# Optimization experiments

Measured on AMD Instinct MI355X. Metric: run time of the kernel, lower is better.

The kernel has to match this reference:

```python
import jax, jax.numpy as jnp
import numpy as np

N = 4096      # (num_domains+1) * batch_size
F_IN = 512    # nfeat
HID = 64      # nhid per head
H = 8         # nheads
ALPHA = 0.2   # leaky-relu negative slope
EDGE_P = 0.01 # adjacency density


def setup_inputs() -> dict:
    key = jax.random.key(0)
    k1, k2, k3, k4 = jax.random.split(key, 4)
    x = jax.random.normal(k1, (N, F_IN), dtype=jnp.float32)
    adj = (jax.random.uniform(k2, (N, N)) < EDGE_P).astype(jnp.float32)
    # ensure self-loops so every row has at least one valid edge for softmax
    adj = jnp.maximum(adj, jnp.eye(N, dtype=jnp.float32))
    W = jax.random.normal(k3, (H, F_IN, HID), dtype=jnp.float32) * 0.1
    a = jax.random.normal(k4, (H, 2 * HID), dtype=jnp.float32) * 0.1
    return {"x": x, "adj": adj, "W": W, "a": a}


def reference(x, adj, W, a):
    # Wh: [H, N, HID] -- per-head linear projection
    Wh = jnp.einsum('nf,hfd->hnd', x, W)
    # additive attention logits: e_ij = leakyrelu(a1.Wh_i + a2.Wh_j)
    e_src = jnp.einsum('hnd,hd->hn', Wh, a[:, :HID])   # [H, N]
    e_dst = jnp.einsum('hnd,hd->hn', Wh, a[:, HID:])   # [H, N]
    e = jax.nn.leaky_relu(e_src[:, :, None] + e_dst[:, None, :], ALPHA)  # [H, N, N]
    e = jnp.where(adj[None] > 0, e, jnp.float32(-9e15))
    att = jax.nn.softmax(e, axis=-1)                    # masked softmax over neighbors
    h = jnp.einsum('hnm,hmd->hnd', att, Wh)             # [H, N, HID]
    h = jax.nn.elu(h)                                   # concat=True -> elu per head
    # concat heads: [N, H*HID]
    return jnp.transpose(h, (1, 0, 2)).reshape(N, H * HID)
```

## Files before the change

kernel.cpp:

```cpp
#include <hip/hip_runtime.h>
#include <hip/hip_bf16.h>
#include <math.h>

#define N_NODES 4096
#define F_IN    512
#define HID     64
#define H       8
#define NJ      512
#define ALPHA   0.2f

typedef __bf16 bf16x8 __attribute__((ext_vector_type(8)));
typedef float  f32x4  __attribute__((ext_vector_type(4)));

#define B_UNITS (NJ * F_IN)

__global__ __launch_bounds__(256) void conv_w(const float* __restrict__ W,
                                              __bf16* __restrict__ Bth) {
    int bid = blockIdx.x * 256 + threadIdx.x;
    int k = bid & (F_IN - 1);
    int j = bid >> 9;
    float v = W[(size_t)(j >> 6) * F_IN * HID + (size_t)k * HID + (j & 63)];
    Bth[(size_t)j * F_IN + k] = (__bf16)v;
}

__global__ __launch_bounds__(256) void wh_gemm_fused(const float* __restrict__ x,
                                                     const __bf16* __restrict__ Bth,
                                                     const float* __restrict__ a,
                                                     __bf16* __restrict__ Whb,
                                                     float* __restrict__ esrc,
                                                     float* __restrict__ edst) {
    const int bid = blockIdx.x;
    const int xcd = bid & 7;
    const int s0  = bid >> 3;
    const int bm  = xcd * 8 + (s0 >> 3);
    const int h   = s0 & 7;

    const int tid  = threadIdx.x;
    const int wave = tid >> 6;
    const int lane = tid & 63;
    const int lm = lane & 15;
    const int lq = lane >> 4;

    __shared__ __align__(16) __bf16 As_h[64][72];
    __shared__ __align__(16) __bf16 As_l[64][72];
    __shared__ __align__(16) __bf16 Bs_h[64][72];

    f32x4 acc[4];
    #pragma unroll
    for (int c = 0; c < 4; c++) acc[c] = (f32x4){0.f, 0.f, 0.f, 0.f};

    for (int k0 = 0; k0 < F_IN; k0 += 64) {
        #pragma unroll
        for (int s = 0; s < 2; s++) {
            int idx = tid + s * 256;
            int m  = idx >> 3;
            int kk = (idx & 7) << 3;
            const float4* gp = (const float4*)(x + (size_t)(bm * 64 + m) * F_IN + k0 + kk);
            float4 v0 = gp[0];
            float4 v1 = gp[1];
            float vv[8] = {v0.x, v0.y, v0.z, v0.w, v1.x, v1.y, v1.z, v1.w};
            bf16x8 hv, lv;
            #pragma unroll
            for (int e = 0; e < 8; e++) {
                __bf16 hi = (__bf16)vv[e];
                hv[e] = hi;
                lv[e] = (__bf16)(vv[e] - (float)hi);
            }
            *(bf16x8*)&As_h[m][kk] = hv;
            *(bf16x8*)&As_l[m][kk] = lv;
            *(uint4*)&Bs_h[m][kk] = *(const uint4*)(Bth + (size_t)(h * 64 + m) * F_IN + k0 + kk);
        }
        __syncthreads();

        #pragma unroll
        for (int kh = 0; kh < 2; kh++) {
            bf16x8 afh = *(const bf16x8*)&As_h[wave * 16 + lm][kh * 32 + lq * 8];
            bf16x8 afl = *(const bf16x8*)&As_l[wave * 16 + lm][kh * 32 + lq * 8];
            bf16x8 bh[4];
            #pragma unroll
            for (int c = 0; c < 4; c++) {
                bh[c] = *(const bf16x8*)&Bs_h[c * 16 + lm][kh * 32 + lq * 8];
            }
            #pragma unroll
            for (int c = 0; c < 4; c++) {
                acc[c] = __builtin_amdgcn_mfma_f32_16x16x32_bf16(afh, bh[c], acc[c], 0, 0, 0);
                acc[c] = __builtin_amdgcn_mfma_f32_16x16x32_bf16(afl, bh[c], acc[c], 0, 0, 0);
            }
        }
        __syncthreads();
    }

    float a1c[4], a2c[4];
    #pragma unroll
    for (int c = 0; c < 4; c++) {
        a1c[c] = a[h * 2 * HID + c * 16 + lm];
        a2c[c] = a[h * 2 * HID + HID + c * 16 + lm];
    }

    #pragma unroll
    for (int r = 0; r < 4; r++) {
        int row = bm * 64 + wave * 16 + lq * 4 + r;
        float s1 = 0.f, s2 = 0.f;
        #pragma unroll
        for (int c = 0; c < 4; c++) {
            float v = acc[c][r];
            Whb[(size_t)row * NJ + h * HID + c * 16 + lm] = (__bf16)v;
            s1 += v * a1c[c];
            s2 += v * a2c[c];
        }
        #pragma unroll
        for (int o = 1; o < 16; o <<= 1) {
            s1 += __shfl_xor(s1, o);
            s2 += __shfl_xor(s2, o);
        }
        if (lm == 0) {
            esrc[h * N_NODES + row] = s1;
            edst[h * N_NODES + row] = s2;
        }
    }
}

#define MAXN 128

__global__ __launch_bounds__(256) void gat_attn(const float* __restrict__ adj,
                                                const __bf16* __restrict__ Whb,
                                                const float* __restrict__ esrc,
                                                const float* __restrict__ edst,
                                                float* __restrict__ out) {
    const int i    = blockIdx.x;
    const int tid  = threadIdx.x;
    const int wave = tid >> 6;
    const int lane = tid & 63;
    __shared__ int    nbr[MAXN];
    __shared__ __align__(8)  float2 an[H][MAXN + 4];
    __shared__ float  denom[H];
    __shared__ __align__(16) f32x4 part[3][2][64];
    __shared__ int    cnt;

    if (tid == 0) cnt = 0;
    __syncthreads();

    const unsigned long long lt = (1ull << lane) - 1ull;
    const f32x4* arow = (const f32x4*)(adj + (size_t)i * N_NODES);
    f32x4 q[4];
    #pragma unroll
    for (int cc = 0; cc < 4; cc++) q[cc] = __builtin_nontemporal_load(arow + cc * 256 + tid);
    #pragma unroll
    for (int cc = 0; cc < 4; cc++) {
        unsigned long long b0 = __ballot(q[cc][0] > 0.f);
        unsigned long long b1 = __ballot(q[cc][1] > 0.f);
        unsigned long long b2 = __ballot(q[cc][2] > 0.f);
        unsigned long long b3 = __ballot(q[cc][3] > 0.f);
        int c0 = __popcll(b0), c1 = __popcll(b1), c2 = __popcll(b2), c3 = __popcll(b3);
        int base = 0;
        if (lane == 0) base = atomicAdd(&cnt, c0 + c1 + c2 + c3);
        base = __shfl(base, 0);
        int col = (cc * 256 + tid) * 4;
        if (q[cc][0] > 0.f) nbr[base + __popcll(b0 & lt)] = col;
        base += c0;
        if (q[cc][1] > 0.f) nbr[base + __popcll(b1 & lt)] = col + 1;
        base += c1;
        if (q[cc][2] > 0.f) nbr[base + __popcll(b2 & lt)] = col + 2;
        base += c2;
        if (q[cc][3] > 0.f) nbr[base + __popcll(b3 & lt)] = col + 3;
    }
    __syncthreads();
    const int n = cnt;

    #pragma unroll
    for (int k = 0; k < 2; k++) {
        const int hh = wave * 2 + k;
        float es = esrc[hh * N_NODES + i];
        float m = -1e30f;
        for (int j = lane; j < n; j += 64) {
            int c = nbr[j];
            float lg = es + edst[hh * N_NODES + c];
            lg = lg > 0.f ? lg : ALPHA * lg;
            an[hh][j] = make_float2(lg, __int_as_float(c << 10));
            m = fmaxf(m, lg);
        }
        #pragma unroll
        for (int o = 32; o; o >>= 1) m = fmaxf(m, __shfl_xor(m, o));
        float s = 0.f;
        for (int j = lane; j < n; j += 64) {
            float w = __expf(an[hh][j].x - m);
            an[hh][j].x = w;
            s += w;
        }
        #pragma unroll
        for (int o = 32; o; o >>= 1) s += __shfl_xor(s, o);
        if (lane == 0) denom[hh] = s;
    }
    __syncthreads();

    const int qd = tid >> 6;
    const int t  = tid & 63;
    const int h  = t >> 3;
    const char* wp = (const char*)Whb + t * 16;
    float a0 = 0.f, a1 = 0.f, a2 = 0.f, a3 = 0.f;
    float a4 = 0.f, a5 = 0.f, a6 = 0.f, a7 = 0.f;
    #pragma unroll 4
    for (int j = qd; j < n; j += 4) {
        float2 p = an[h][j];
        uint4 u = *(const uint4*)(wp + __float_as_uint(p.y));
        float w = p.x;
        a0 += w * __uint_as_float(u.x << 16);
        a1 += w * __uint_as_float(u.x & 0xffff0000u);
        a2 += w * __uint_as_float(u.y << 16);
        a3 += w * __uint_as_float(u.y & 0xffff0000u);
        a4 += w * __uint_as_float(u.z << 16);
        a5 += w * __uint_as_float(u.z & 0xffff0000u);
        a6 += w * __uint_as_float(u.w << 16);
        a7 += w * __uint_as_float(u.w & 0xffff0000u);
    }
    if (qd) {
        part[qd - 1][0][t] = (f32x4){a0, a1, a2, a3};
        part[qd - 1][1][t] = (f32x4){a4, a5, a6, a7};
    }
    __syncthreads();
    if (qd == 0) {
        f32x4 r0 = (f32x4){a0, a1, a2, a3};
        f32x4 r1 = (f32x4){a4, a5, a6, a7};
        #pragma unroll
        for (int s = 0; s < 3; s++) {
            r0 += part[s][0][t];
            r1 += part[s][1][t];
        }
        float inv = 1.f / denom[h];
        float b[8];
        #pragma unroll
        for (int e = 0; e < 4; e++) b[e] = r0[e] * inv;
        #pragma unroll
        for (int e = 0; e < 4; e++) b[4 + e] = r1[e] * inv;
        #pragma unroll
        for (int e = 0; e < 8; e++) b[e] = b[e] > 0.f ? b[e] : expm1f(b[e]);
        f32x4 o0 = (f32x4){b[0], b[1], b[2], b[3]};
        f32x4 o1 = (f32x4){b[4], b[5], b[6], b[7]};
        f32x4* op = (f32x4*)(out + (size_t)i * NJ + t * 8);
        __builtin_nontemporal_store(o0, op);
        __builtin_nontemporal_store(o1, op + 1);
    }
}

extern "C" void kernel_launch(void* const* d_in, const int* in_sizes, int n_in,
                              void* d_out, int out_size, void* d_ws, size_t ws_size,
                              hipStream_t stream) {
    const float* x   = (const float*)d_in[0];
    const float* adj = (const float*)d_in[1];
    const float* W   = (const float*)d_in[2];
    const float* a   = (const float*)d_in[3];
    float* out = (float*)d_out;

    float*  esrc = (float*)d_ws;
    float*  edst = esrc + (size_t)H * N_NODES;
    __bf16* Whb  = (__bf16*)(edst + (size_t)H * N_NODES);
    __bf16* Bth  = Whb + (size_t)N_NODES * NJ;

    conv_w<<<B_UNITS / 256, 256, 0, stream>>>(W, Bth);

    wh_gemm_fused<<<512, 256, 0, stream>>>(x, Bth, a, Whb, esrc, edst);

    gat_attn<<<N_NODES, 256, 0, stream>>>(adj, Whb, esrc, edst, out);
}
```

Before: 135.4 us.

## Pre-tile and swizzle bf16 hi/lo operands, load GEMM tiles via async global-to-LDS

The fp32→bf16 hi/lo split of x moves out of the GEMM into a prep kernel, which also transposes W. The prep kernel writes both operands in a pre-tiled, XOR-swizzled layout. The GEMM then fills LDS with direct global_load_lds 16-byte copies and reads fragments through the matching swizzle instead of using padded rows. This removes the per-block conversion of x, which was repeated for each of the 8 heads. The cost is an extra write and read of two N×F bf16 arrays through global memory.

```diff
diff --git a/kernel.cpp b/kernel.cpp
--- a/kernel.cpp
+++ b/kernel.cpp
@@ -12,23 +12,65 @@
 typedef __bf16 bf16x8 __attribute__((ext_vector_type(8)));
 typedef float  f32x4  __attribute__((ext_vector_type(4)));
 
-#define B_UNITS (NJ * F_IN)
-
-__global__ __launch_bounds__(256) void conv_w(const float* __restrict__ W,
-                                              __bf16* __restrict__ Bth) {
-    int bid = blockIdx.x * 256 + threadIdx.x;
-    int k = bid & (F_IN - 1);
-    int j = bid >> 9;
-    float v = W[(size_t)(j >> 6) * F_IN * HID + (size_t)k * HID + (j & 63)];
-    Bth[(size_t)j * F_IN + k] = (__bf16)v;
-}
-
-__global__ __launch_bounds__(256) void wh_gemm_fused(const float* __restrict__ x,
-                                                     const __bf16* __restrict__ Bth,
-                                                     const float* __restrict__ a,
-                                                     __bf16* __restrict__ Whb,
-                                                     float* __restrict__ esrc,
-                                                     float* __restrict__ edst) {
+#define A_CHUNKS (N_NODES * F_IN / 8)
+#define B_CHUNKS (NJ * F_IN / 8)
+
+__global__ __launch_bounds__(256) void conv_prep(const float* __restrict__ x,
+                                                 const float* __restrict__ W,
+                                                 __bf16* __restrict__ AhT,
+                                                 __bf16* __restrict__ AlT,
+                                                 __bf16* __restrict__ BthT) {
+    int id = blockIdx.x * 256 + threadIdx.x;
+    if (id < A_CHUNKS) {
+        int u  = id & 511;
+        int kt = (id >> 9) & 7;
+        int bm = id >> 12;
+        int r  = u >> 3, c8 = u & 7;
+        int col = kt * 64 + ((c8 ^ (r & 7)) << 3);
+        const float4* gp = (const float4*)(x + (size_t)(bm * 64 + r) * F_IN + col);
+        float4 v0 = gp[0];
+        float4 v1 = gp[1];
+        float vv[8] = {v0.x, v0.y, v0.z, v0.w, v1.x, v1.y, v1.z, v1.w};
+        bf16x8 hv, lv;
+        #pragma unroll
+        for (int e = 0; e < 8; e++) {
+            __bf16 hi = (__bf16)vv[e];
+            hv[e] = hi;
+            lv[e] = (__bf16)(vv[e] - (float)hi);
+        }
+        *(bf16x8*)(AhT + (size_t)id * 8) = hv;
+        *(bf16x8*)(AlT + (size_t)id * 8) = lv;
+    } else {
+        int bid = id - A_CHUNKS;
+        if (bid < B_CHUNKS) {
+            int u  = bid & 511;
+            int kt = (bid >> 9) & 7;
+            int h  = bid >> 12;
+            int r  = u >> 3, c8 = u & 7;
+            int kb = kt * 64 + ((c8 ^ (r & 7)) << 3);
+            bf16x8 hv;
+            #pragma unroll
+            for (int e = 0; e < 8; e++) {
+                hv[e] = (__bf16)W[((size_t)h * F_IN + kb + e) * HID + r];
+            }
+            *(bf16x8*)(BthT + (size_t)bid * 8) = hv;
+        }
+    }
+}
+
+__device__ __forceinline__ void async16(void* lds, const void* g) {
+    __builtin_amdgcn_global_load_lds(
+        (const __attribute__((address_space(1))) unsigned int*)g,
+        (__attribute__((address_space(3))) unsigned int*)lds, 16, 0, 0);
+}
+
+__global__ __launch_bounds__(256) void wh_gemm(const __bf16* __restrict__ AhT,
+                                               const __bf16* __restrict__ AlT,
+                                               const __bf16* __restrict__ BthT,
+                                               const float* __restrict__ a,
+                                               __bf16* __restrict__ Whb,
+                                               float* __restrict__ esrc,
+                                               float* __restrict__ edst) {
     const int bid = blockIdx.x;
     const int xcd = bid & 7;
     const int s0  = bid >> 3;
@@ -41,45 +83,42 @@
     const int lm = lane & 15;
     const int lq = lane >> 4;
 
-    __shared__ __align__(16) __bf16 As_h[64][72];
-    __shared__ __align__(16) __bf16 As_l[64][72];
-    __shared__ __align__(16) __bf16 Bs_h[64][72];
+    __shared__ __align__(16) __bf16 smem[3 * 4096];
+    __bf16* Ash = smem;
+    __bf16* Asl = smem + 4096;
+    __bf16* Bsh = smem + 8192;
 
     f32x4 acc[4];
     #pragma unroll
     for (int c = 0; c < 4; c++) acc[c] = (f32x4){0.f, 0.f, 0.f, 0.f};
 
-    for (int k0 = 0; k0 < F_IN; k0 += 64) {
+    const __bf16* tA_h = AhT  + (size_t)bm * (8 * 4096);
+    const __bf16* tA_l = AlT  + (size_t)bm * (8 * 4096);
+    const __bf16* tB   = BthT + (size_t)h  * (8 * 4096);
+
+    const int rowA = wave * 16 + lm;
+
+    for (int kt = 0; kt < 8; kt++) {
+        const size_t ko = (size_t)kt * 4096;
         #pragma unroll
         for (int s = 0; s < 2; s++) {
-            int idx = tid + s * 256;
-            int m  = idx >> 3;
-            int kk = (idx & 7) << 3;
-            const float4* gp = (const float4*)(x + (size_t)(bm * 64 + m) * F_IN + k0 + kk);
-            float4 v0 = gp[0];
-            float4 v1 = gp[1];
-            float vv[8] = {v0.x, v0.y, v0.z, v0.w, v1.x, v1.y, v1.z, v1.w};
-            bf16x8 hv, lv;
-            #pragma unroll
-            for (int e = 0; e < 8; e++) {
-                __bf16 hi = (__bf16)vv[e];
-                hv[e] = hi;
-                lv[e] = (__bf16)(vv[e] - (float)hi);
-            }
-            *(bf16x8*)&As_h[m][kk] = hv;
-            *(bf16x8*)&As_l[m][kk] = lv;
-            *(uint4*)&Bs_h[m][kk] = *(const uint4*)(Bth + (size_t)(h * 64 + m) * F_IN + k0 + kk);
+            int u  = s * 256 + tid;
+            int ub = s * 256 + wave * 64;
+            async16(Ash + ub * 8, tA_h + ko + (size_t)u * 8);
+            async16(Asl + ub * 8, tA_l + ko + (size_t)u * 8);
+            async16(Bsh + ub * 8, tB   + ko + (size_t)u * 8);
         }
         __syncthreads();
 
         #pragma unroll
         for (int kh = 0; kh < 2; kh++) {
-            bf16x8 afh = *(const bf16x8*)&As_h[wave * 16 + lm][kh * 32 + lq * 8];
-            bf16x8 afl = *(const bf16x8*)&As_l[wave * 16 + lm][kh * 32 + lq * 8];
+            const int ce = (((kh << 2) + lq) ^ (lm & 7)) << 3;
+            bf16x8 afh = *(const bf16x8*)&Ash[rowA * 64 + ce];
+            bf16x8 afl = *(const bf16x8*)&Asl[rowA * 64 + ce];
             bf16x8 bh[4];
             #pragma unroll
             for (int c = 0; c < 4; c++) {
-                bh[c] = *(const bf16x8*)&Bs_h[c * 16 + lm][kh * 32 + lq * 8];
+                bh[c] = *(const bf16x8*)&Bsh[(c * 16 + lm) * 64 + ce];
             }
             #pragma unroll
             for (int c = 0; c < 4; c++) {
@@ -254,11 +293,13 @@
     float*  esrc = (float*)d_ws;
     float*  edst = esrc + (size_t)H * N_NODES;
     __bf16* Whb  = (__bf16*)(edst + (size_t)H * N_NODES);
-    __bf16* Bth  = Whb + (size_t)N_NODES * NJ;
-
-    conv_w<<<B_UNITS / 256, 256, 0, stream>>>(W, Bth);
-
-    wh_gemm_fused<<<512, 256, 0, stream>>>(x, Bth, a, Whb, esrc, edst);
+    __bf16* AhT  = Whb + (size_t)N_NODES * NJ;
+    __bf16* AlT  = AhT + (size_t)N_NODES * F_IN;
+    __bf16* BthT = AlT + (size_t)N_NODES * F_IN;
+
+    conv_prep<<<(A_CHUNKS + B_CHUNKS) / 256, 256, 0, stream>>>(x, W, AhT, AlT, BthT);
+
+    wh_gemm<<<512, 256, 0, stream>>>(AhT, AlT, BthT, a, Whb, esrc, edst);
 
     gat_attn<<<N_NODES, 256, 0, stream>>>(adj, Whb, esrc, edst, out);
 }
```

Result: no change. 135.8 us (+0.2%).
